# Performance work log

Measured on AMD Instinct MI355X. Metric: run time of the kernel, lower is better.

Reference implementation:

```python
import jax, jax.numpy as jnp
import numpy as np

POWERS = (0, 1, 2)
IN_F, OUT_F = 64, 64
B, N, T = 8, 2048, 12


def setup_inputs() -> dict:
    key = jax.random.key(0)
    ks = jax.random.split(key, 8)
    inp = {
        "x": jax.random.normal(ks[0], (B, IN_F, N, T), dtype=jnp.float32),
        "adj": jax.random.uniform(ks[1], (B, N, N), dtype=jnp.float32),
    }
    # Xavier-uniform weights per adjacency power, zero biases (as in initialize_weights)
    limit = float(np.sqrt(6.0 / (IN_F + OUT_F)))
    for i, p in enumerate(POWERS):
        inp[f"W{p}"] = jax.random.uniform(ks[2 + i], (IN_F, OUT_F), jnp.float32, -limit, limit)
        inp[f"b{p}"] = jnp.zeros((OUT_F,), jnp.float32)
    return inp


def _gcn_conv(x, adj, W, b, a_power):
    # x: [B, F, N, T]; W: [F, O]; adj: [B, N, N]
    h = jnp.einsum('bfnt,fo->bont', x, W) + b[None, :, None, None]
    # repeated diffusion along node axis: h[f, n] <- sum_m adj[n, m] h[f, m]
    for _ in range(a_power):
        h = jnp.einsum('bnm,bomt->bont', adj, h)
    return jax.nn.leaky_relu(h)  # default negative_slope 0.01, same as torch


def reference(x, adj, W0, b0, W1, b1, W2, b2):
    params = {0: (W0, b0), 1: (W1, b1), 2: (W2, b2)}
    outs = [_gcn_conv(x, adj, params[p][0], params[p][1], p) for p in POWERS]
    return jnp.concatenate(outs, axis=1)  # [B, len(POWERS)*O, N, T]
```

## Files before the change

kernel.cpp:

```cpp
#include <hip/hip_runtime.h>

#define B_ 8
#define N_ 2048
#define T_ 12
#define F_ 64
#define NT 24576
#define CH 192
#define C_ 768

typedef __bf16 bf16x8 __attribute__((ext_vector_type(8)));
typedef float f32x4 __attribute__((ext_vector_type(4)));

typedef const __attribute__((address_space(1))) unsigned int as1_uint;
typedef __attribute__((address_space(3))) unsigned int as3_uint;

__device__ __forceinline__ void gload16(const void* g, void* l) {
  __builtin_amdgcn_global_load_lds((as1_uint*)g, (as3_uint*)l, 16, 0, 0);
}

__device__ __forceinline__ unsigned short f2bf(float f) {
  unsigned int u = __float_as_uint(f);
  u += 0x7FFFu + ((u >> 16) & 1u);
  return (unsigned short)(u >> 16);
}

__device__ __forceinline__ float leaky(float v) {
  return v >= 0.0f ? v : 0.01f * v;
}

__global__ __launch_bounds__(256) void convert_adj_k(const float* __restrict__ adj,
                                                     unsigned short* __restrict__ adjb) {
  size_t i = (size_t)blockIdx.x * 256 + threadIdx.x;
  const float4 v = reinterpret_cast<const float4*>(adj)[i];
  ushort4 u;
  u.x = f2bf(v.x); u.y = f2bf(v.y); u.z = f2bf(v.z); u.w = f2bf(v.w);
  reinterpret_cast<ushort4*>(adjb)[i] = u;
}

__device__ __forceinline__ void stage_wt(const float* __restrict__ W,
                                         unsigned short* Wt, int tid) {
  const int f = tid >> 2;
  const int q = tid & 3;
  const float4* row = reinterpret_cast<const float4*>(W + f * 64 + q * 16);
#pragma unroll
  for (int v4 = 0; v4 < 4; ++v4) {
    float4 v = row[v4];
    const int ob = q * 16 + v4 * 4;
    Wt[(ob + 0) * 72 + f] = f2bf(v.x);
    Wt[(ob + 1) * 72 + f] = f2bf(v.y);
    Wt[(ob + 2) * 72 + f] = f2bf(v.z);
    Wt[(ob + 3) * 72 + f] = f2bf(v.w);
  }
}

__global__ __launch_bounds__(256) void p0_k(const float* __restrict__ x,
                                            const float* __restrict__ W0,
                                            const float* __restrict__ bia0,
                                            float* __restrict__ out) {
  __shared__ unsigned short Wt[64 * 72];
  __shared__ float bias[64];
  const int tid = threadIdx.x;
  stage_wt(W0, Wt, tid);
  if (tid < 64) bias[tid] = bia0[tid];
  __syncthreads();

  const int lane = tid & 63;
  const int wave = tid >> 6;
  const int b = blockIdx.y;
  const int e = blockIdx.x * 64 + wave * 16 + (lane & 15);
  const int fgrp = (lane >> 4) * 8;
  const float* xb = x + (size_t)b * F_ * NT;

  bf16x8 xf[2];
#pragma unroll
  for (int kf = 0; kf < 2; ++kf)
#pragma unroll
    for (int j = 0; j < 8; ++j)
      xf[kf][j] = (__bf16)xb[(size_t)(fgrp + kf * 32 + j) * NT + e];

  float* outb = out + (size_t)b * CH * NT;
#pragma unroll
  for (int ob = 0; ob < 4; ++ob) {
    f32x4 acc = {};
#pragma unroll
    for (int kf = 0; kf < 2; ++kf) {
      bf16x8 af = *reinterpret_cast<const bf16x8*>(
          &Wt[(ob * 16 + (lane & 15)) * 72 + kf * 32 + fgrp]);
      acc = __builtin_amdgcn_mfma_f32_16x16x32_bf16(af, xf[kf], acc, 0, 0, 0);
    }
#pragma unroll
    for (int r = 0; r < 4; ++r) {
      const int o = ob * 16 + (lane >> 4) * 4 + r;
      outb[(size_t)o * NT + e] = leaky(acc[r] + bias[o]);
    }
  }
}

__global__ __launch_bounds__(256) void p12_k(const float* __restrict__ x,
                                             const float* __restrict__ W1,
                                             const float* __restrict__ bia1,
                                             const float* __restrict__ W2,
                                             const float* __restrict__ bia2,
                                             unsigned short* __restrict__ G1,
                                             unsigned short* __restrict__ G2) {
  __shared__ unsigned short Wt[2][64 * 72];
  __shared__ float bias[2][64];
  const int tid = threadIdx.x;
  stage_wt(W1, Wt[0], tid);
  stage_wt(W2, Wt[1], tid);
  if (tid < 64) bias[0][tid] = bia1[tid];
  else if (tid < 128) bias[1][tid - 64] = bia2[tid - 64];
  __syncthreads();

  const int lane = tid & 63;
  const int wave = tid >> 6;
  const int b = blockIdx.y;
  const int n = blockIdx.x * 16 + (lane & 15);
  const int fgrp = (lane >> 4) * 8;
  const float* xb = x + (size_t)b * F_ * NT;
  unsigned short* Gp[2] = {G1 + (size_t)b * C_ * N_, G2 + (size_t)b * C_ * N_};

#pragma unroll
  for (int it = 0; it < 3; ++it) {
    const int t = wave * 3 + it;
    const int e = n * T_ + t;

    bf16x8 xf[2];
#pragma unroll
    for (int kf = 0; kf < 2; ++kf)
#pragma unroll
      for (int j = 0; j < 8; ++j)
        xf[kf][j] = (__bf16)xb[(size_t)(fgrp + kf * 32 + j) * NT + e];

#pragma unroll
    for (int p = 0; p < 2; ++p) {
#pragma unroll
      for (int ob = 0; ob < 4; ++ob) {
        f32x4 acc = {};
#pragma unroll
        for (int kf = 0; kf < 2; ++kf) {
          bf16x8 af = *reinterpret_cast<const bf16x8*>(
              &Wt[p][(ob * 16 + (lane & 15)) * 72 + kf * 32 + fgrp]);
          acc = __builtin_amdgcn_mfma_f32_16x16x32_bf16(af, xf[kf], acc, 0, 0, 0);
        }
#pragma unroll
        for (int r = 0; r < 4; ++r) {
          const int o = ob * 16 + (lane >> 4) * 4 + r;
          Gp[p][(size_t)(o * T_ + t) * N_ + n] = f2bf(acc[r] + bias[p][o]);
        }
      }
    }
  }
}

__global__ __launch_bounds__(512, 2) void gemm8_k(
    const unsigned short* __restrict__ adjb,
    const unsigned short* __restrict__ Bt,
    float* __restrict__ out,
    unsigned short* __restrict__ Ht,
    const int mode, const int ochan_base)
{
  extern __shared__ __align__(16) unsigned short lds[];

  const int tid  = threadIdx.x;
  const int lane = tid & 63;
  const int wave = tid >> 6;
  const int wr = wave >> 2;
  const int wc = wave & 3;

  const int b  = blockIdx.x & 7;
  const int w  = blockIdx.x >> 3;
  const int n0 = (w & 7) * 256;
  const int c0 = (w >> 3) * 192;

  const unsigned short* A  = adjb + (size_t)b * N_ * N_;
  const unsigned short* Bm = Bt   + (size_t)b * C_ * N_;

  const int swzSrc = ((lane & 3) ^ ((lane >> 3) & 3)) * 8;
  const unsigned short* aSt1 = A + (size_t)(n0 + wave * 16 + (lane >> 2)) * N_ + swzSrc;
  const unsigned short* aSt2 = aSt1 + (size_t)128 * N_;
  const unsigned short* bSt1 = Bm + (size_t)(c0 + wave * 16 + (lane >> 2)) * N_ + swzSrc;
  const int brow2 = c0 + 128 + wave * 16 + (lane >> 2);
  const unsigned short* bSt2 = Bm + (size_t)(brow2 < C_ ? brow2 : C_ - 1) * N_ + swzSrc;
  const int ldsW = wave * 512;

  const int kg  = (lane >> 4) ^ ((lane >> 1) & 3);
  const int aRd = (wr * 128 + (lane & 15)) * 32 + kg * 8;
  const int bRd = (wc * 48  + (lane & 15)) * 32 + kg * 8;

  f32x4 acc[8][3] = {};
  bf16x8 afr0[8], afr1[8], bfr0[3], bfr1[3];

#define STGA(LDSB, KT, KH) \
  gload16(aSt1 + (KT) * 64 + (KH) * 32, lds + (LDSB) + (KH) * 8192 + ldsW); \
  gload16(aSt2 + (KT) * 64 + (KH) * 32, lds + (LDSB) + (KH) * 8192 + ldsW + 4096);

#define STGB(LDSB, KT, KH) \
  gload16(bSt1 + (KT) * 64 + (KH) * 32, lds + (LDSB) + (KH) * 8192 + ldsW); \
  gload16(bSt2 + (KT) * 64 + (KH) * 32, lds + (LDSB) + (KH) * 8192 + ldsW + 4096);

#define RD_B(SET, BUFB, KH) { \
  _Pragma("unroll") \
  for (int nf = 0; nf < 3; ++nf) \
    bfr##SET[nf] = *(const bf16x8*)(lds + (BUFB) + (KH) * 8192 + nf * 512 + bRd); }

#define RD_A8(SET, BUFA, KH) { \
  _Pragma("unroll") \
  for (int mm = 0; mm < 8; ++mm) \
    afr##SET[mm] = *(const bf16x8*)(lds + (BUFA) + (KH) * 8192 + mm * 512 + aRd); }

#define MFMA24(SET) { \
  _Pragma("unroll") \
  for (int mm = 0; mm < 8; ++mm) \
  _Pragma("unroll") \
  for (int nf = 0; nf < 3; ++nf) \
    acc[mm][nf] = __builtin_amdgcn_mfma_f32_16x16x32_bf16( \
        afr##SET[mm], bfr##SET[nf], acc[mm][nf], 0, 0, 0); }

#define WAITV_(N) asm volatile("s_waitcnt vmcnt(" #N ")" ::: "memory");
#define WAITV(N) WAITV_(N)

#define PHASE(SETC, SETN, BUFN, KHN, STBUF, STKT, STKH) \
  STGA(STBUF, STKT, STKH) STGB((STBUF) + 32768, STKT, STKH) \
  WAITV(8) \
  __builtin_amdgcn_s_barrier(); \
  RD_B(SETN, (BUFN) + 32768, KHN) RD_A8(SETN, BUFN, KHN) \
  __builtin_amdgcn_sched_barrier(0); \
  __builtin_amdgcn_s_setprio(1); \
  MFMA24(SETC) \
  __builtin_amdgcn_s_setprio(0); \
  __builtin_amdgcn_s_barrier();

#define PHASE_NOST(SETC, SETN, BUFN, KHN, WVN) \
  WAITV(WVN) \
  __builtin_amdgcn_s_barrier(); \
  RD_B(SETN, (BUFN) + 32768, KHN) RD_A8(SETN, BUFN, KHN) \
  __builtin_amdgcn_sched_barrier(0); \
  __builtin_amdgcn_s_setprio(1); \
  MFMA24(SETC) \
  __builtin_amdgcn_s_setprio(0); \
  __builtin_amdgcn_s_barrier();

  STGA(0, 0, 0)      STGB(32768, 0, 0)
  STGA(0, 0, 1)      STGB(32768, 0, 1)
  STGA(16384, 1, 0)  STGB(49152, 1, 0)
  WAITV(8)
  __builtin_amdgcn_s_barrier();
  RD_B(0, 32768, 0) RD_A8(0, 0, 0)

#pragma unroll 1
  for (int it = 0; it < 15; ++it) {
    const int kt2 = 2 * it;
    PHASE(0, 1, 0, 1, 16384, kt2 + 1, 1)
    PHASE(1, 0, 16384, 0, 0, kt2 + 2, 0)
    PHASE(0, 1, 16384, 1, 0, kt2 + 2, 1)
    PHASE(1, 0, 0, 0, 16384, kt2 + 3, 0)
  }

  PHASE(0, 1, 0, 1, 16384, 31, 1)
  PHASE_NOST(1, 0, 16384, 0, 4)
  PHASE_NOST(0, 1, 16384, 1, 0)
  __builtin_amdgcn_s_barrier();
  __builtin_amdgcn_s_setprio(1);
  MFMA24(1)
  __builtin_amdgcn_s_setprio(0);

  const int r4 = (lane >> 4) * 4;
  if (mode == 0) {
    float* outb = out + (size_t)b * CH * NT;
#pragma unroll
    for (int m = 0; m < 8; ++m) {
#pragma unroll
      for (int nf = 0; nf < 3; ++nf) {
        const int c = c0 + wc * 48 + nf * 16 + (lane & 15);
        const int o = c / 12;
        const int t = c - o * 12;
#pragma unroll
        for (int r = 0; r < 4; ++r) {
          const int n = n0 + wr * 128 + m * 16 + r4 + r;
          outb[((size_t)(ochan_base + o) * N_ + n) * T_ + t] = leaky(acc[m][nf][r]);
        }
      }
    }
  } else {
    unsigned short* Hb = Ht + (size_t)b * C_ * N_;
#pragma unroll
    for (int m = 0; m < 8; ++m) {
#pragma unroll
      for (int nf = 0; nf < 3; ++nf) {
        const int c = c0 + wc * 48 + nf * 16 + (lane & 15);
        const int nb = n0 + wr * 128 + m * 16 + r4;
        ushort4 u;
        u.x = f2bf(acc[m][nf][0]);
        u.y = f2bf(acc[m][nf][1]);
        u.z = f2bf(acc[m][nf][2]);
        u.w = f2bf(acc[m][nf][3]);
        *reinterpret_cast<ushort4*>(&Hb[(size_t)c * N_ + nb]) = u;
      }
    }
  }
#undef STGA
#undef STGB
#undef RD_B
#undef RD_A8
#undef MFMA24
#undef PHASE
#undef PHASE_NOST
#undef WAITV
#undef WAITV_
}

extern "C" void kernel_launch(void* const* d_in, const int* in_sizes, int n_in,
                              void* d_out, int out_size, void* d_ws, size_t ws_size,
                              hipStream_t stream) {
  const float* x   = (const float*)d_in[0];
  const float* adj = (const float*)d_in[1];
  const float* W0  = (const float*)d_in[2];
  const float* b0  = (const float*)d_in[3];
  const float* W1  = (const float*)d_in[4];
  const float* b1  = (const float*)d_in[5];
  const float* W2  = (const float*)d_in[6];
  const float* b2  = (const float*)d_in[7];
  float* out = (float*)d_out;

  char* ws = (char*)d_ws;
  unsigned short* adjb = (unsigned short*)ws;
  unsigned short* G1   = (unsigned short*)(ws + 67108864);
  unsigned short* G2   = (unsigned short*)(ws + 92274688);
  unsigned short* Ht   = G1;

  hipFuncSetAttribute((const void*)gemm8_k,
                      hipFuncAttributeMaxDynamicSharedMemorySize, 131072);

  hipLaunchKernelGGL(convert_adj_k, dim3((B_ * N_ * N_ / 4) / 256), dim3(256), 0, stream,
                     adj, adjb);

  hipLaunchKernelGGL(p0_k, dim3(NT / 64, B_), dim3(256), 0, stream,
                     x, W0, b0, out);

  hipLaunchKernelGGL(p12_k, dim3(N_ / 16, B_), dim3(256), 0, stream,
                     x, W1, b1, W2, b2, G1, G2);

  hipLaunchKernelGGL(gemm8_k, dim3(256), dim3(512), 131072, stream,
                     adjb, G1, out, (unsigned short*)nullptr, 0, 64);

  hipLaunchKernelGGL(gemm8_k, dim3(256), dim3(512), 131072, stream,
                     adjb, G2, out, Ht, 1, 0);

  hipLaunchKernelGGL(gemm8_k, dim3(256), dim3(512), 131072, stream,
                     adjb, Ht, out, (unsigned short*)nullptr, 0, 128);
}
```

Measured before the change: 282.2 us.

## Shrink GEMM tile to 128x192 with 4 waves and triple-buffered K=32 slots

Restructures the adjacency GEMM from 256x192 tiles with 8 waves and 128KB of dynamic LDS to 128x192 tiles with 4 waves, using a 3-slot static LDS ring of K=32 stages (about 60KB). The grid doubles to 512 blocks, aiming to fill more CUs and let two blocks co-reside, and the pipeline now keeps two stages in flight. In exchange, each block gets less A/B reuse, and the shorter K steps mean more barriers per unit of work.

```diff
diff --git a/kernel.cpp b/kernel.cpp
--- a/kernel.cpp
+++ b/kernel.cpp
@@ -153,61 +153,58 @@
   }
 }
 
-__global__ __launch_bounds__(512, 2) void gemm8_k(
+#define SLOTSZ 10240
+
+__global__ __launch_bounds__(256, 2) void gemm8_k(
     const unsigned short* __restrict__ adjb,
     const unsigned short* __restrict__ Bt,
     float* __restrict__ out,
     unsigned short* __restrict__ Ht,
     const int mode, const int ochan_base)
 {
-  extern __shared__ __align__(16) unsigned short lds[];
+  __shared__ __align__(16) unsigned short lds[3][SLOTSZ];
 
   const int tid  = threadIdx.x;
   const int lane = tid & 63;
   const int wave = tid >> 6;
-  const int wr = wave >> 2;
-  const int wc = wave & 3;
+  const int wc = wave;
 
   const int b  = blockIdx.x & 7;
-  const int w  = blockIdx.x >> 3;
-  const int n0 = (w & 7) * 256;
-  const int c0 = (w >> 3) * 192;
+  const int j  = blockIdx.x >> 3;
+  const int n0 = (j & 15) * 128;
+  const int c0 = (j >> 4) * 192;
 
   const unsigned short* A  = adjb + (size_t)b * N_ * N_;
   const unsigned short* Bm = Bt   + (size_t)b * C_ * N_;
 
   const int swzSrc = ((lane & 3) ^ ((lane >> 3) & 3)) * 8;
-  const unsigned short* aSt1 = A + (size_t)(n0 + wave * 16 + (lane >> 2)) * N_ + swzSrc;
-  const unsigned short* aSt2 = aSt1 + (size_t)128 * N_;
-  const unsigned short* bSt1 = Bm + (size_t)(c0 + wave * 16 + (lane >> 2)) * N_ + swzSrc;
-  const int brow2 = c0 + 128 + wave * 16 + (lane >> 2);
-  const unsigned short* bSt2 = Bm + (size_t)(brow2 < C_ ? brow2 : C_ - 1) * N_ + swzSrc;
-  const int ldsW = wave * 512;
+  const unsigned short* aS0 = A + (size_t)(n0 + wave * 32 +  0 + (lane >> 2)) * N_ + swzSrc;
+  const unsigned short* aS1 = A + (size_t)(n0 + wave * 32 + 16 + (lane >> 2)) * N_ + swzSrc;
+  const unsigned short* bS0 = Bm + (size_t)(c0 + wave * 48 +  0 + (lane >> 2)) * N_ + swzSrc;
+  const unsigned short* bS1 = Bm + (size_t)(c0 + wave * 48 + 16 + (lane >> 2)) * N_ + swzSrc;
+  const unsigned short* bS2 = Bm + (size_t)(c0 + wave * 48 + 32 + (lane >> 2)) * N_ + swzSrc;
 
   const int kg  = (lane >> 4) ^ ((lane >> 1) & 3);
-  const int aRd = (wr * 128 + (lane & 15)) * 32 + kg * 8;
-  const int bRd = (wc * 48  + (lane & 15)) * 32 + kg * 8;
+  const int rdL = (lane & 15) * 32 + kg * 8;
+  const int bOff = 4096 + wc * 1536;
 
   f32x4 acc[8][3] = {};
   bf16x8 afr0[8], afr1[8], bfr0[3], bfr1[3];
 
-#define STGA(LDSB, KT, KH) \
-  gload16(aSt1 + (KT) * 64 + (KH) * 32, lds + (LDSB) + (KH) * 8192 + ldsW); \
-  gload16(aSt2 + (KT) * 64 + (KH) * 32, lds + (LDSB) + (KH) * 8192 + ldsW + 4096);
-
-#define STGB(LDSB, KT, KH) \
-  gload16(bSt1 + (KT) * 64 + (KH) * 32, lds + (LDSB) + (KH) * 8192 + ldsW); \
-  gload16(bSt2 + (KT) * 64 + (KH) * 32, lds + (LDSB) + (KH) * 8192 + ldsW + 4096);
-
-#define RD_B(SET, BUFB, KH) { \
+#define STG(S, KT) \
+  gload16(aS0 + (KT) * 32, &lds[S][wave * 1024]); \
+  gload16(aS1 + (KT) * 32, &lds[S][wave * 1024 + 512]); \
+  gload16(bS0 + (KT) * 32, &lds[S][4096 + wave * 1536]); \
+  gload16(bS1 + (KT) * 32, &lds[S][4096 + wave * 1536 + 512]); \
+  gload16(bS2 + (KT) * 32, &lds[S][4096 + wave * 1536 + 1024]);
+
+#define RD(SET, S) { \
   _Pragma("unroll") \
   for (int nf = 0; nf < 3; ++nf) \
-    bfr##SET[nf] = *(const bf16x8*)(lds + (BUFB) + (KH) * 8192 + nf * 512 + bRd); }
-
-#define RD_A8(SET, BUFA, KH) { \
+    bfr##SET[nf] = *(const bf16x8*)(&lds[S][bOff + nf * 512 + rdL]); \
   _Pragma("unroll") \
   for (int mm = 0; mm < 8; ++mm) \
-    afr##SET[mm] = *(const bf16x8*)(lds + (BUFA) + (KH) * 8192 + mm * 512 + aRd); }
+    afr##SET[mm] = *(const bf16x8*)(&lds[S][mm * 512 + rdL]); }
 
 #define MFMA24(SET) { \
   _Pragma("unroll") \
@@ -220,46 +217,45 @@
 #define WAITV_(N) asm volatile("s_waitcnt vmcnt(" #N ")" ::: "memory");
 #define WAITV(N) WAITV_(N)
 
-#define PHASE(SETC, SETN, BUFN, KHN, STBUF, STKT, STKH) \
-  STGA(STBUF, STKT, STKH) STGB((STBUF) + 32768, STKT, STKH) \
-  WAITV(8) \
+#define PHASE(SETC, SETN, SN, SS, KT) \
+  STG(SS, KT) \
+  WAITV(5) \
   __builtin_amdgcn_s_barrier(); \
-  RD_B(SETN, (BUFN) + 32768, KHN) RD_A8(SETN, BUFN, KHN) \
+  RD(SETN, SN) \
   __builtin_amdgcn_sched_barrier(0); \
   __builtin_amdgcn_s_setprio(1); \
   MFMA24(SETC) \
+  __builtin_amdgcn_sched_barrier(0); \
   __builtin_amdgcn_s_setprio(0); \
   __builtin_amdgcn_s_barrier();
 
-#define PHASE_NOST(SETC, SETN, BUFN, KHN, WVN) \
-  WAITV(WVN) \
-  __builtin_amdgcn_s_barrier(); \
-  RD_B(SETN, (BUFN) + 32768, KHN) RD_A8(SETN, BUFN, KHN) \
-  __builtin_amdgcn_sched_barrier(0); \
-  __builtin_amdgcn_s_setprio(1); \
-  MFMA24(SETC) \
-  __builtin_amdgcn_s_setprio(0); \
+  STG(0, 0)
+  STG(1, 1)
+  WAITV(5)
   __builtin_amdgcn_s_barrier();
-
-  STGA(0, 0, 0)      STGB(32768, 0, 0)
-  STGA(0, 0, 1)      STGB(32768, 0, 1)
-  STGA(16384, 1, 0)  STGB(49152, 1, 0)
-  WAITV(8)
+  RD(0, 0)
+
+#pragma unroll 1
+  for (int it = 0; it < 10; ++it) {
+    const int kt = 6 * it;
+    PHASE(0, 1, 1, 2, kt + 2)
+    PHASE(1, 0, 2, 0, kt + 3)
+    PHASE(0, 1, 0, 1, kt + 4)
+    PHASE(1, 0, 1, 2, kt + 5)
+    PHASE(0, 1, 2, 0, kt + 6)
+    PHASE(1, 0, 0, 1, kt + 7)
+  }
+
+  PHASE(0, 1, 1, 2, 62)
+  PHASE(1, 0, 2, 0, 63)
+  WAITV(0)
   __builtin_amdgcn_s_barrier();
-  RD_B(0, 32768, 0) RD_A8(0, 0, 0)
-
-#pragma unroll 1
-  for (int it = 0; it < 15; ++it) {
-    const int kt2 = 2 * it;
-    PHASE(0, 1, 0, 1, 16384, kt2 + 1, 1)
-    PHASE(1, 0, 16384, 0, 0, kt2 + 2, 0)
-    PHASE(0, 1, 16384, 1, 0, kt2 + 2, 1)
-    PHASE(1, 0, 0, 0, 16384, kt2 + 3, 0)
-  }
-
-  PHASE(0, 1, 0, 1, 16384, 31, 1)
-  PHASE_NOST(1, 0, 16384, 0, 4)
-  PHASE_NOST(0, 1, 16384, 1, 0)
+  RD(1, 0)
+  __builtin_amdgcn_sched_barrier(0);
+  __builtin_amdgcn_s_setprio(1);
+  MFMA24(0)
+  __builtin_amdgcn_sched_barrier(0);
+  __builtin_amdgcn_s_setprio(0);
   __builtin_amdgcn_s_barrier();
   __builtin_amdgcn_s_setprio(1);
   MFMA24(1)
@@ -277,7 +273,7 @@
         const int t = c - o * 12;
 #pragma unroll
         for (int r = 0; r < 4; ++r) {
-          const int n = n0 + wr * 128 + m * 16 + r4 + r;
+          const int n = n0 + m * 16 + r4 + r;
           outb[((size_t)(ochan_base + o) * N_ + n) * T_ + t] = leaky(acc[m][nf][r]);
         }
       }
@@ -289,7 +285,7 @@
 #pragma unroll
       for (int nf = 0; nf < 3; ++nf) {
         const int c = c0 + wc * 48 + nf * 16 + (lane & 15);
-        const int nb = n0 + wr * 128 + m * 16 + r4;
+        const int nb = n0 + m * 16 + r4;
         ushort4 u;
         u.x = f2bf(acc[m][nf][0]);
         u.y = f2bf(acc[m][nf][1]);
@@ -299,13 +295,10 @@
       }
     }
   }
-#undef STGA
-#undef STGB
-#undef RD_B
-#undef RD_A8
+#undef STG
+#undef RD
 #undef MFMA24
 #undef PHASE
-#undef PHASE_NOST
 #undef WAITV
 #undef WAITV_
 }
@@ -329,9 +322,6 @@
   unsigned short* G2   = (unsigned short*)(ws + 92274688);
   unsigned short* Ht   = G1;
 
-  hipFuncSetAttribute((const void*)gemm8_k,
-                      hipFuncAttributeMaxDynamicSharedMemorySize, 131072);
-
   hipLaunchKernelGGL(convert_adj_k, dim3((B_ * N_ * N_ / 4) / 256), dim3(256), 0, stream,
                      adj, adjb);
 
@@ -341,12 +331,12 @@
   hipLaunchKernelGGL(p12_k, dim3(N_ / 16, B_), dim3(256), 0, stream,
                      x, W1, b1, W2, b2, G1, G2);
 
-  hipLaunchKernelGGL(gemm8_k, dim3(256), dim3(512), 131072, stream,
+  hipLaunchKernelGGL(gemm8_k, dim3(512), dim3(256), 0, stream,
                      adjb, G1, out, (unsigned short*)nullptr, 0, 64);
 
-  hipLaunchKernelGGL(gemm8_k, dim3(256), dim3(512), 131072, stream,
+  hipLaunchKernelGGL(gemm8_k, dim3(512), dim3(256), 0, stream,
                      adjb, G2, out, Ht, 1, 0);
 
-  hipLaunchKernelGGL(gemm8_k, dim3(256), dim3(512), 131072, stream,
+  hipLaunchKernelGGL(gemm8_k, dim3(512), dim3(256), 0, stream,
                      adjb, Ht, out, (unsigned short*)nullptr, 0, 128);
 }
```

Result: no change. 285.5 us (+1.2%).
